# Kernel optimization log

Hardware: AMD Instinct MI355X
Metric: run time of the kernel (lower is better)

Reference implementation:

```python
import jax, jax.numpy as jnp
import numpy as np

B, N, E = 4, 2048, 512
H = 8
HD = E // H  # 64
SCALE = HD ** -0.5


def setup_inputs() -> dict:
    key = jax.random.key(0)
    k1, k2, k3 = jax.random.split(key, 3)
    x = jax.random.normal(k1, (B, N, E), dtype=jnp.float32)
    # xavier-uniform-like scaling for weights
    w_qkv = jax.random.normal(k2, (3 * E, E), dtype=jnp.float32) * (2.0 / (4 * E)) ** 0.5
    b_qkv = jnp.zeros((3 * E,), dtype=jnp.float32)
    w_out = jax.random.normal(k3, (E, E), dtype=jnp.float32) * (1.0 / E) ** 0.5
    b_out = jnp.zeros((E,), dtype=jnp.float32)
    return {"x": x, "w_qkv": w_qkv, "b_qkv": b_qkv, "w_out": w_out, "b_out": b_out}


def reference(x, w_qkv, b_qkv, w_out, b_out):
    b_sz, n_patches, _ = x.shape
    # qkv projection: [B,N,3E] -> [B,N,3,H,HD] -> [B,H,3,N,HD]
    qkv = (jnp.einsum('bne,fe->bnf', x, w_qkv) + b_qkv)
    qkv = qkv.reshape(b_sz, n_patches, 3, H, HD).transpose(0, 3, 2, 1, 4)
    q, k, v = qkv[:, :, 0], qkv[:, :, 1], qkv[:, :, 2]  # each [B,H,N,HD]
    attn = jnp.einsum('bhqd,bhkd->bhqk', q * SCALE, k)  # [B,H,N,N]
    attn = jax.nn.softmax(attn, axis=-1)
    # attn_dropout p=0.0 -> identity in reference
    out = jnp.einsum('bhqk,bhkd->bhqd', attn, v)  # [B,H,N,HD]
    out = out.transpose(0, 2, 1, 3).reshape(b_sz, n_patches, E)
    out = jnp.einsum('bne,fe->bnf', out, w_out) + b_out
    return out
```

## Files before the change

kernel.cpp:

```cpp
#include <hip/hip_runtime.h>

#define BB   4
#define SEQ  2048
#define EMB  512
#define NH   8
#define HD   64
#define QSCALE 0.18033688011f

typedef __bf16 bf16x8 __attribute__((ext_vector_type(8)));
typedef float  f32x4  __attribute__((ext_vector_type(4)));

__device__ __forceinline__ short f2bf(float f) {
  union { float f; unsigned u; } v; v.f = f;
  unsigned r = v.u + 0x7fffu + ((v.u >> 16) & 1u);
  return (short)(r >> 16);
}

__device__ __forceinline__ unsigned pk_bf16(float a, float b) {
#if __has_builtin(__builtin_amdgcn_cvt_pk_bf16_f32)
  typedef __bf16 bf16v2 __attribute__((ext_vector_type(2)));
  union { bf16v2 v; unsigned u; } cv;
  cv.v = __builtin_amdgcn_cvt_pk_bf16_f32(a, b);
  return cv.u;
#else
  return (unsigned)(unsigned short)f2bf(a) | ((unsigned)(unsigned short)f2bf(b) << 16);
#endif
}

__device__ __forceinline__ float fexp2(float x) {
#if __has_builtin(__builtin_amdgcn_exp2f)
  return __builtin_amdgcn_exp2f(x);
#else
  return exp2f(x);
#endif
}

__device__ __forceinline__ void gl_lds16(const void* g, void* l) {
  __builtin_amdgcn_global_load_lds(
      (const __attribute__((address_space(1))) unsigned int*)g,
      (__attribute__((address_space(3))) unsigned int*)l, 16, 0, 0);
}

__device__ __forceinline__ void quad_redist(unsigned &a, unsigned &b) {
  asm volatile("v_permlane32_swap_b32 %0, %1" : "+v"(a), "+v"(b));
  asm volatile("v_permlane16_swap_b32 %0, %1" : "+v"(a), "+v"(b));
}

__global__ __launch_bounds__(256) void cast_all(const float* __restrict__ x,
                                                const float* __restrict__ wq,
                                                const float* __restrict__ wo,
                                                short* __restrict__ xb,
                                                short* __restrict__ wqb,
                                                short* __restrict__ wob) {
  int i = blockIdx.x * 256 + threadIdx.x;
  const float* src; short* dst; int off;
  if (i < 1048576)      { src = x;  dst = xb;  off = i; }
  else if (i < 1245184) { src = wq; dst = wqb; off = i - 1048576; }
  else                  { src = wo; dst = wob; off = i - 1245184; }
  float4 v = ((const float4*)src)[off];
  uint2 o; o.x = pk_bf16(v.x, v.y); o.y = pk_bf16(v.z, v.w);
  *(uint2*)&dst[off * 4] = o;
}

__global__ __launch_bounds__(512, 6) void qkv_gemm(const short* __restrict__ A,
                                                   const short* __restrict__ W,
                                                   const float* __restrict__ bias,
                                                   short* __restrict__ qo,
                                                   short* __restrict__ ko,
                                                   short* __restrict__ vto) {
  __shared__ __align__(16) short As0[128 * 32];
  __shared__ __align__(16) short Bs0[128 * 32];
  __shared__ __align__(16) short As1[128 * 32];
  __shared__ __align__(16) short Bs1[128 * 32];
  const int tid  = threadIdx.x;
  const int lane = tid & 63, wave = tid >> 6;
  const int wm = wave >> 1, wf = wave & 1;
  const int col = lane & 15, quad = lane >> 4;
  const int m0 = blockIdx.x * 128, f0 = blockIdx.y * 128;

  const int row = tid >> 2;
  const int cb  = (tid & 3) ^ ((tid >> 3) & 3);
  const short* aSrc = A + (size_t)(m0 + row) * 512 + cb * 8;
  const short* wSrc = W + (size_t)(f0 + row) * 512 + cb * 8;

  const int rc = (quad ^ ((col >> 1) & 3)) * 8;
  int aOff[2], bOff[4];
#pragma unroll
  for (int i = 0; i < 2; ++i) aOff[i] = (wm * 32 + i * 16 + col) * 32 + rc;
#pragma unroll
  for (int j = 0; j < 4; ++j) bOff[j] = (wf * 64 + j * 16 + col) * 32 + rc;

  f32x4 acc[2][4];
#pragma unroll
  for (int i = 0; i < 2; ++i)
#pragma unroll
    for (int j = 0; j < 4; ++j)
#pragma unroll
      for (int r = 0; r < 4; ++r) acc[i][j][r] = 0.f;

#define QSTAGE(BUFA, BUFB, KS)                                        \
  {                                                                   \
    gl_lds16(aSrc + (KS) * 32, (char*)(BUFA) + wave * 1024);          \
    gl_lds16(wSrc + (KS) * 32, (char*)(BUFB) + wave * 1024);          \
  }

  auto qcompute = [&](const short* As, const short* Bs) {
    bf16x8 af[2], bw[4];
#pragma unroll
    for (int i = 0; i < 2; ++i) af[i] = *(const bf16x8*)&As[aOff[i]];
#pragma unroll
    for (int j = 0; j < 4; ++j) bw[j] = *(const bf16x8*)&Bs[bOff[j]];
#pragma unroll
    for (int i = 0; i < 2; ++i)
#pragma unroll
      for (int j = 0; j < 4; ++j)
        acc[i][j] = __builtin_amdgcn_mfma_f32_16x16x32_bf16(af[i], bw[j], acc[i][j], 0, 0, 0);
  };

  QSTAGE(As0, Bs0, 0);
  __syncthreads();
  for (int t = 0; t < 16; t += 2) {
    QSTAGE(As1, Bs1, t + 1);
    qcompute(As0, Bs0);
    __syncthreads();
    QSTAGE(As0, Bs0, (t + 2) & 15);
    qcompute(As1, Bs1);
    __syncthreads();
  }
#undef QSTAGE

#pragma unroll
  for (int j = 0; j < 4; ++j) {
    const int f = f0 + wf * 64 + j * 16 + col;
    const float bv = bias[f];
    const int sIdx = f >> 9;
    const int h = (f >> 6) & 7;
    const int d = f & 63;
#pragma unroll
    for (int i = 0; i < 2; ++i) {
      const int mbase = m0 + wm * 32 + i * 16 + quad * 4;
      const int b = mbase >> 11;
      const int n = mbase & 2047;
      const size_t bh = (size_t)(b * NH + h);
      if (sIdx == 2) {
        uint2 pk;
        pk.x = pk_bf16(acc[i][j][0] + bv, acc[i][j][1] + bv);
        pk.y = pk_bf16(acc[i][j][2] + bv, acc[i][j][3] + bv);
        *(uint2*)&vto[(bh * HD + d) * SEQ + n] = pk;
      } else if (sIdx == 0) {
#pragma unroll
        for (int r = 0; r < 4; ++r)
          qo[(bh * SEQ + n + r) * HD + d] = f2bf((acc[i][j][r] + bv) * QSCALE);
      } else {
#pragma unroll
        for (int r = 0; r < 4; ++r)
          ko[(bh * SEQ + n + r) * HD + d] = f2bf(acc[i][j][r] + bv);
      }
    }
  }
}

__global__ __launch_bounds__(512) void attn_kernel(const short* __restrict__ q,
                                                   const short* __restrict__ k,
                                                   const short* __restrict__ vt,
                                                   short* __restrict__ o) {
  __shared__ __align__(16) short Ks0[64 * 64];
  __shared__ __align__(16) short Vs0[64 * 64];
  __shared__ __align__(16) short Ks1[64 * 64];
  __shared__ __align__(16) short Vs1[64 * 64];

  const int tid  = threadIdx.x;
  const int lane = tid & 63, wave = tid >> 6;
  const int col = lane & 15, quad = lane >> 4;
  const int bh = blockIdx.x & 31;
  const int q0 = (blockIdx.x >> 5) * 128;
  const size_t bhBase = (size_t)bh * SEQ * HD;

  bf16x8 qf[2];
#pragma unroll
  for (int ks = 0; ks < 2; ++ks)
    qf[ks] = *(const bf16x8*)&q[bhBase +
        (size_t)(q0 + wave * 16 + col) * HD + ks * 32 + quad * 8];

  const int row = tid >> 3, cb = (tid & 7) ^ (row & 7);
  const short* ksrc = k  + bhBase + (size_t)row * HD  + cb * 8;
  const short* vsrc = vt + bhBase + (size_t)row * SEQ + cb * 8;
  char* const ldsK0 = (char*)Ks0 + wave * 1024;
  char* const ldsV0 = (char*)Vs0 + wave * 1024;
  char* const ldsK1 = (char*)Ks1 + wave * 1024;
  char* const ldsV1 = (char*)Vs1 + wave * 1024;

  f32x4 oacc[4];
#pragma unroll
  for (int nt = 0; nt < 4; ++nt)
#pragma unroll
    for (int r = 0; r < 4; ++r) oacc[nt][r] = 0.f;
  float lsum = 0.f;

  auto compute = [&](const short* KB, const short* VB) {
    f32x4 sacc[4];
#pragma unroll
    for (int kt = 0; kt < 4; ++kt)
#pragma unroll
      for (int r = 0; r < 4; ++r) sacc[kt][r] = 0.f;
#pragma unroll
    for (int ks = 0; ks < 2; ++ks)
#pragma unroll
      for (int kt = 0; kt < 4; ++kt) {
        bf16x8 kf = *(const bf16x8*)&KB[(kt * 16 + col) * 64 +
                                        (((ks * 4 + quad) ^ (col & 7)) * 8)];
        sacc[kt] = __builtin_amdgcn_mfma_f32_16x16x32_bf16(kf, qf[ks], sacc[kt], 0, 0, 0);
      }

    unsigned u[4][2];
#pragma unroll
    for (int kt = 0; kt < 4; ++kt) {
      float p0 = fexp2(sacc[kt][0]);
      float p1 = fexp2(sacc[kt][1]);
      float p2 = fexp2(sacc[kt][2]);
      float p3 = fexp2(sacc[kt][3]);
      lsum += (p0 + p1) + (p2 + p3);
      u[kt][0] = pk_bf16(p0, p1);
      u[kt][1] = pk_bf16(p2, p3);
    }

    union { unsigned w[4]; bf16x8 v; } pf0, pf1;
    {
      unsigned a, b;
      a = u[0][0]; b = u[1][0]; quad_redist(a, b); pf0.w[0] = a; pf0.w[2] = b;
      a = u[0][1]; b = u[1][1]; quad_redist(a, b); pf0.w[1] = a; pf0.w[3] = b;
      a = u[2][0]; b = u[3][0]; quad_redist(a, b); pf1.w[0] = a; pf1.w[2] = b;
      a = u[2][1]; b = u[3][1]; quad_redist(a, b); pf1.w[1] = a; pf1.w[3] = b;
    }

#pragma unroll
    for (int nt = 0; nt < 4; ++nt) {
      bf16x8 vf0 = *(const bf16x8*)&VB[(nt * 16 + col) * 64 +
                                       ((quad ^ (col & 7)) * 8)];
      oacc[nt] = __builtin_amdgcn_mfma_f32_16x16x32_bf16(pf0.v, vf0, oacc[nt], 0, 0, 0);
      bf16x8 vf1 = *(const bf16x8*)&VB[(nt * 16 + col) * 64 +
                                       (((4 + quad) ^ (col & 7)) * 8)];
      oacc[nt] = __builtin_amdgcn_mfma_f32_16x16x32_bf16(pf1.v, vf1, oacc[nt], 0, 0, 0);
    }
  };

  gl_lds16(ksrc, ldsK0); gl_lds16(vsrc, ldsV0);
  ksrc += 64 * HD; vsrc += 64;
  __syncthreads();

  for (int t = 0; t < 32; t += 2) {
    gl_lds16(ksrc, ldsK1); gl_lds16(vsrc, ldsV1);
    ksrc += 64 * HD; vsrc += 64;
    compute(Ks0, Vs0);
    __syncthreads();
    gl_lds16(ksrc, ldsK0); gl_lds16(vsrc, ldsV0);
    ksrc += 64 * HD; vsrc += 64;
    compute(Ks1, Vs1);
    __syncthreads();
  }

  lsum += __shfl_xor(lsum, 16);
  lsum += __shfl_xor(lsum, 32);

  const int b = bh >> 3, h = bh & 7;
#pragma unroll
  for (int r = 0; r < 4; ++r) {
    const float rl = 1.0f / __shfl(lsum, quad * 4 + r);
    const int n = q0 + wave * 16 + quad * 4 + r;
#pragma unroll
    for (int nt = 0; nt < 4; ++nt)
      o[((size_t)(b * SEQ + n)) * EMB + h * HD + nt * 16 + col] = f2bf(oacc[nt][r] * rl);
  }
}

__global__ __launch_bounds__(512, 4) void proj_gemm(const short* __restrict__ A,
                                                    const short* __restrict__ W,
                                                    const float* __restrict__ bias,
                                                    float* __restrict__ out) {
  __shared__ __align__(16) short As0[64 * 32];
  __shared__ __align__(16) short Bs0[128 * 32];
  __shared__ __align__(16) short As1[64 * 32];
  __shared__ __align__(16) short Bs1[128 * 32];
  const int tid  = threadIdx.x;
  const int lane = tid & 63, wave = tid >> 6;
  const int wm = wave >> 2, wf = wave & 3;
  const int col = lane & 15, quad = lane >> 4;
  const int m0 = blockIdx.x * 64, f0 = blockIdx.y * 128;

  const int aslot = tid & 255;
  const int arow = aslot >> 2, acb = (aslot & 3) ^ ((aslot >> 3) & 3);
  const short* aSrc = A + (size_t)(m0 + arow) * 512 + acb * 8;
  const int wrow = tid >> 2, wcb = (tid & 3) ^ ((tid >> 3) & 3);
  const short* wSrc = W + (size_t)(f0 + wrow) * 512 + wcb * 8;

  const int rc = (quad ^ ((col >> 1) & 3)) * 8;
  int aOff[2], bOff[2];
#pragma unroll
  for (int i = 0; i < 2; ++i) aOff[i] = (wm * 32 + i * 16 + col) * 32 + rc;
#pragma unroll
  for (int j = 0; j < 2; ++j) bOff[j] = (wf * 32 + j * 16 + col) * 32 + rc;

  f32x4 acc[2][2];
#pragma unroll
  for (int i = 0; i < 2; ++i)
#pragma unroll
    for (int j = 0; j < 2; ++j)
#pragma unroll
      for (int r = 0; r < 4; ++r) acc[i][j][r] = 0.f;

#define PSTAGE(BUFA, BUFB, KS)                                        \
  {                                                                   \
    if (wave < 4) gl_lds16(aSrc + (KS) * 32, (char*)(BUFA) + wave * 1024); \
    gl_lds16(wSrc + (KS) * 32, (char*)(BUFB) + wave * 1024);          \
  }

  auto pcompute = [&](const short* As, const short* Bs) {
    bf16x8 af[2], bw[2];
#pragma unroll
    for (int i = 0; i < 2; ++i) af[i] = *(const bf16x8*)&As[aOff[i]];
#pragma unroll
    for (int j = 0; j < 2; ++j) bw[j] = *(const bf16x8*)&Bs[bOff[j]];
#pragma unroll
    for (int i = 0; i < 2; ++i)
#pragma unroll
      for (int j = 0; j < 2; ++j)
        acc[i][j] = __builtin_amdgcn_mfma_f32_16x16x32_bf16(af[i], bw[j], acc[i][j], 0, 0, 0);
  };

  PSTAGE(As0, Bs0, 0);
  __syncthreads();
  for (int t = 0; t < 16; t += 2) {
    PSTAGE(As1, Bs1, t + 1);
    pcompute(As0, Bs0);
    __syncthreads();
    PSTAGE(As0, Bs0, (t + 2) & 15);
    pcompute(As1, Bs1);
    __syncthreads();
  }
#undef PSTAGE

#pragma unroll
  for (int j = 0; j < 2; ++j) {
    const int f = f0 + wf * 32 + j * 16 + col;
    const float bv = bias[f];
#pragma unroll
    for (int i = 0; i < 2; ++i) {
      const int mbase = m0 + wm * 32 + i * 16 + quad * 4;
#pragma unroll
      for (int r = 0; r < 4; ++r)
        out[(size_t)(mbase + r) * 512 + f] = acc[i][j][r] + bv;
    }
  }
}

extern "C" void kernel_launch(void* const* d_in, const int* in_sizes, int n_in,
                              void* d_out, int out_size, void* d_ws, size_t ws_size,
                              hipStream_t stream) {
  (void)in_sizes; (void)n_in; (void)out_size; (void)ws_size;
  const float* x     = (const float*)d_in[0];
  const float* w_qkv = (const float*)d_in[1];
  const float* b_qkv = (const float*)d_in[2];
  const float* w_out = (const float*)d_in[3];
  const float* b_out = (const float*)d_in[4];
  float* out = (float*)d_out;

  char* ws = (char*)d_ws;
  short* xb    = (short*)(ws + 0);
  short* wqkvb = (short*)(ws + 8388608);
  short* woutb = (short*)(ws + 9961472);
  short* qb    = (short*)(ws + 10485760);
  short* kb    = (short*)(ws + 18874368);
  short* vtb   = (short*)(ws + 27262976);
  short* ob    = (short*)(ws + 35651584);

  cast_all<<<5120, 256, 0, stream>>>(x, w_qkv, w_out, xb, wqkvb, woutb);
  qkv_gemm<<<dim3(64, 12), 512, 0, stream>>>(xb, wqkvb, b_qkv, qb, kb, vtb);
  attn_kernel<<<512, 512, 0, stream>>>(qb, kb, vtb, ob);
  proj_gemm<<<dim3(128, 4), 512, 0, stream>>>(ob, woutb, b_out, out);
}
```

Measured before the change: 153.8 us.

## Triple-buffer LDS in QKV and projection GEMMs with vmcnt-based waits

Replaces the double-buffered K loop in the qkv and output-projection GEMMs with a three-stage ring of LDS buffers. Two stages are prefetched, and each iteration waits only on the oldest outstanding global-to-LDS loads via explicit s_waitcnt vmcnt, then uses a single s_barrier. This keeps more loads in flight and drops one barrier per step. In exchange it uses more LDS per block, which may lower occupancy, and it depends on exact vmcnt bookkeeping for correctness.

```diff
diff --git a/kernel.cpp b/kernel.cpp
--- a/kernel.cpp
+++ b/kernel.cpp
@@ -68,10 +68,8 @@
                                                    short* __restrict__ qo,
                                                    short* __restrict__ ko,
                                                    short* __restrict__ vto) {
-  __shared__ __align__(16) short As0[128 * 32];
-  __shared__ __align__(16) short Bs0[128 * 32];
-  __shared__ __align__(16) short As1[128 * 32];
-  __shared__ __align__(16) short Bs1[128 * 32];
+  __shared__ __align__(16) short As[3][128 * 32];
+  __shared__ __align__(16) short Bs[3][128 * 32];
   const int tid  = threadIdx.x;
   const int lane = tid & 63, wave = tid >> 6;
   const int wm = wave >> 1, wf = wave & 1;
@@ -98,18 +96,18 @@
 #pragma unroll
       for (int r = 0; r < 4; ++r) acc[i][j][r] = 0.f;
 
-#define QSTAGE(BUFA, BUFB, KS)                                        \
+#define QSTAGE(BI, KS)                                                \
   {                                                                   \
-    gl_lds16(aSrc + (KS) * 32, (char*)(BUFA) + wave * 1024);          \
-    gl_lds16(wSrc + (KS) * 32, (char*)(BUFB) + wave * 1024);          \
-  }
-
-  auto qcompute = [&](const short* As, const short* Bs) {
+    gl_lds16(aSrc + (KS) * 32, (char*)As[BI] + wave * 1024);          \
+    gl_lds16(wSrc + (KS) * 32, (char*)Bs[BI] + wave * 1024);          \
+  }
+
+  auto qcompute = [&](const short* Asb, const short* Bsb) {
     bf16x8 af[2], bw[4];
 #pragma unroll
-    for (int i = 0; i < 2; ++i) af[i] = *(const bf16x8*)&As[aOff[i]];
-#pragma unroll
-    for (int j = 0; j < 4; ++j) bw[j] = *(const bf16x8*)&Bs[bOff[j]];
+    for (int i = 0; i < 2; ++i) af[i] = *(const bf16x8*)&Asb[aOff[i]];
+#pragma unroll
+    for (int j = 0; j < 4; ++j) bw[j] = *(const bf16x8*)&Bsb[bOff[j]];
 #pragma unroll
     for (int i = 0; i < 2; ++i)
 #pragma unroll
@@ -117,15 +115,16 @@
         acc[i][j] = __builtin_amdgcn_mfma_f32_16x16x32_bf16(af[i], bw[j], acc[i][j], 0, 0, 0);
   };
 
-  QSTAGE(As0, Bs0, 0);
-  __syncthreads();
-  for (int t = 0; t < 16; t += 2) {
-    QSTAGE(As1, Bs1, t + 1);
-    qcompute(As0, Bs0);
-    __syncthreads();
-    QSTAGE(As0, Bs0, (t + 2) & 15);
-    qcompute(As1, Bs1);
-    __syncthreads();
+  QSTAGE(0, 0);
+  QSTAGE(1, 1);
+#pragma unroll
+  for (int t = 0; t < 16; ++t) {
+    if (t < 15) { asm volatile("s_waitcnt vmcnt(2)" ::: "memory"); }
+    else        { asm volatile("s_waitcnt vmcnt(0)" ::: "memory"); }
+    __builtin_amdgcn_sched_barrier(0);
+    __builtin_amdgcn_s_barrier();
+    if (t + 2 < 16) QSTAGE((t + 2) % 3, t + 2);
+    qcompute(As[t % 3], Bs[t % 3]);
   }
 #undef QSTAGE
 
@@ -277,10 +276,8 @@
                                                     const short* __restrict__ W,
                                                     const float* __restrict__ bias,
                                                     float* __restrict__ out) {
-  __shared__ __align__(16) short As0[64 * 32];
-  __shared__ __align__(16) short Bs0[128 * 32];
-  __shared__ __align__(16) short As1[64 * 32];
-  __shared__ __align__(16) short Bs1[128 * 32];
+  __shared__ __align__(16) short As[3][64 * 32];
+  __shared__ __align__(16) short Bs[3][128 * 32];
   const int tid  = threadIdx.x;
   const int lane = tid & 63, wave = tid >> 6;
   const int wm = wave >> 2, wf = wave & 3;
@@ -308,18 +305,18 @@
 #pragma unroll
       for (int r = 0; r < 4; ++r) acc[i][j][r] = 0.f;
 
-#define PSTAGE(BUFA, BUFB, KS)                                        \
+#define PSTAGE(BI, KS)                                                \
   {                                                                   \
-    if (wave < 4) gl_lds16(aSrc + (KS) * 32, (char*)(BUFA) + wave * 1024); \
-    gl_lds16(wSrc + (KS) * 32, (char*)(BUFB) + wave * 1024);          \
-  }
-
-  auto pcompute = [&](const short* As, const short* Bs) {
+    if (wave < 4) gl_lds16(aSrc + (KS) * 32, (char*)As[BI] + wave * 1024); \
+    gl_lds16(wSrc + (KS) * 32, (char*)Bs[BI] + wave * 1024);          \
+  }
+
+  auto pcompute = [&](const short* Asb, const short* Bsb) {
     bf16x8 af[2], bw[2];
 #pragma unroll
-    for (int i = 0; i < 2; ++i) af[i] = *(const bf16x8*)&As[aOff[i]];
-#pragma unroll
-    for (int j = 0; j < 2; ++j) bw[j] = *(const bf16x8*)&Bs[bOff[j]];
+    for (int i = 0; i < 2; ++i) af[i] = *(const bf16x8*)&Asb[aOff[i]];
+#pragma unroll
+    for (int j = 0; j < 2; ++j) bw[j] = *(const bf16x8*)&Bsb[bOff[j]];
 #pragma unroll
     for (int i = 0; i < 2; ++i)
 #pragma unroll
@@ -327,15 +324,20 @@
         acc[i][j] = __builtin_amdgcn_mfma_f32_16x16x32_bf16(af[i], bw[j], acc[i][j], 0, 0, 0);
   };
 
-  PSTAGE(As0, Bs0, 0);
-  __syncthreads();
-  for (int t = 0; t < 16; t += 2) {
-    PSTAGE(As1, Bs1, t + 1);
-    pcompute(As0, Bs0);
-    __syncthreads();
-    PSTAGE(As0, Bs0, (t + 2) & 15);
-    pcompute(As1, Bs1);
-    __syncthreads();
+  PSTAGE(0, 0);
+  PSTAGE(1, 1);
+#pragma unroll
+  for (int t = 0; t < 16; ++t) {
+    if (t < 15) {
+      if (wave < 4) { asm volatile("s_waitcnt vmcnt(2)" ::: "memory"); }
+      else          { asm volatile("s_waitcnt vmcnt(1)" ::: "memory"); }
+    } else {
+      asm volatile("s_waitcnt vmcnt(0)" ::: "memory");
+    }
+    __builtin_amdgcn_sched_barrier(0);
+    __builtin_amdgcn_s_barrier();
+    if (t + 2 < 16) PSTAGE((t + 2) % 3, t + 2);
+    pcompute(As[t % 3], Bs[t % 3]);
   }
 #undef PSTAGE
 
```

Result: no change. 155.1 us (+0.9%).

## Switch attention to 32x32x16 MFMA with split-KV waves and LDS reduction

Applied to the files above, without the earlier changes.

Rewrites the attention inner loop to use 32x32x16 bf16 MFMA tiles instead of 16x16x32. Each pair of waves shares a 32-row query group and splits each 64-key tile between them. The partial outputs and row sums are combined through LDS at the end. The aim is fewer MFMA and LDS fragment loads per useful FLOP and simpler permlane redistribution, at the cost of an extra cross-wave reduction and a higher occupancy hint.

```diff
diff --git a/kernel.cpp b/kernel.cpp
--- a/kernel.cpp
+++ b/kernel.cpp
@@ -9,6 +9,7 @@
 
 typedef __bf16 bf16x8 __attribute__((ext_vector_type(8)));
 typedef float  f32x4  __attribute__((ext_vector_type(4)));
+typedef float  f32x16 __attribute__((ext_vector_type(16)));
 
 __device__ __forceinline__ short f2bf(float f) {
   union { float f; unsigned u; } v; v.f = f;
@@ -41,9 +42,8 @@
       (__attribute__((address_space(3))) unsigned int*)l, 16, 0, 0);
 }
 
-__device__ __forceinline__ void quad_redist(unsigned &a, unsigned &b) {
+__device__ __forceinline__ void swap32(unsigned &a, unsigned &b) {
   asm volatile("v_permlane32_swap_b32 %0, %1" : "+v"(a), "+v"(b));
-  asm volatile("v_permlane16_swap_b32 %0, %1" : "+v"(a), "+v"(b));
 }
 
 __global__ __launch_bounds__(256) void cast_all(const float* __restrict__ x,
@@ -160,88 +160,82 @@
   }
 }
 
-__global__ __launch_bounds__(512) void attn_kernel(const short* __restrict__ q,
-                                                   const short* __restrict__ k,
-                                                   const short* __restrict__ vt,
-                                                   short* __restrict__ o) {
-  __shared__ __align__(16) short Ks0[64 * 64];
-  __shared__ __align__(16) short Vs0[64 * 64];
-  __shared__ __align__(16) short Ks1[64 * 64];
-  __shared__ __align__(16) short Vs1[64 * 64];
+__global__ __launch_bounds__(512, 4) void attn_kernel(const short* __restrict__ q,
+                                                      const short* __restrict__ k,
+                                                      const short* __restrict__ vt,
+                                                      short* __restrict__ o) {
+  __shared__ __align__(16) short KV[4][64 * 64];
+  __shared__ float Ls[4][32];
 
   const int tid  = threadIdx.x;
   const int lane = tid & 63, wave = tid >> 6;
-  const int col = lane & 15, quad = lane >> 4;
+  const int l31 = lane & 31, g = lane >> 5;
+  const int qg = wave >> 1, kh = wave & 1;
   const int bh = blockIdx.x & 31;
   const int q0 = (blockIdx.x >> 5) * 128;
   const size_t bhBase = (size_t)bh * SEQ * HD;
 
-  bf16x8 qf[2];
-#pragma unroll
-  for (int ks = 0; ks < 2; ++ks)
+  bf16x8 qf[4];
+#pragma unroll
+  for (int ks = 0; ks < 4; ++ks)
     qf[ks] = *(const bf16x8*)&q[bhBase +
-        (size_t)(q0 + wave * 16 + col) * HD + ks * 32 + quad * 8];
+        (size_t)(q0 + qg * 32 + l31) * HD + ks * 16 + g * 8];
 
   const int row = tid >> 3, cb = (tid & 7) ^ (row & 7);
   const short* ksrc = k  + bhBase + (size_t)row * HD  + cb * 8;
   const short* vsrc = vt + bhBase + (size_t)row * SEQ + cb * 8;
-  char* const ldsK0 = (char*)Ks0 + wave * 1024;
-  char* const ldsV0 = (char*)Vs0 + wave * 1024;
-  char* const ldsK1 = (char*)Ks1 + wave * 1024;
-  char* const ldsV1 = (char*)Vs1 + wave * 1024;
-
-  f32x4 oacc[4];
-#pragma unroll
-  for (int nt = 0; nt < 4; ++nt)
-#pragma unroll
-    for (int r = 0; r < 4; ++r) oacc[nt][r] = 0.f;
+  char* const ldsK0 = (char*)KV[0] + wave * 1024;
+  char* const ldsV0 = (char*)KV[1] + wave * 1024;
+  char* const ldsK1 = (char*)KV[2] + wave * 1024;
+  char* const ldsV1 = (char*)KV[3] + wave * 1024;
+
+  f32x16 oacc[2];
+#pragma unroll
+  for (int nt = 0; nt < 2; ++nt)
+#pragma unroll
+    for (int r = 0; r < 16; ++r) oacc[nt][r] = 0.f;
   float lsum = 0.f;
 
+  const int krow = kh * 32 + l31;
+  const int kx   = krow & 7;
+
   auto compute = [&](const short* KB, const short* VB) {
-    f32x4 sacc[4];
-#pragma unroll
-    for (int kt = 0; kt < 4; ++kt)
-#pragma unroll
-      for (int r = 0; r < 4; ++r) sacc[kt][r] = 0.f;
-#pragma unroll
-    for (int ks = 0; ks < 2; ++ks)
-#pragma unroll
-      for (int kt = 0; kt < 4; ++kt) {
-        bf16x8 kf = *(const bf16x8*)&KB[(kt * 16 + col) * 64 +
-                                        (((ks * 4 + quad) ^ (col & 7)) * 8)];
-        sacc[kt] = __builtin_amdgcn_mfma_f32_16x16x32_bf16(kf, qf[ks], sacc[kt], 0, 0, 0);
-      }
-
+    f32x16 sacc;
+#pragma unroll
+    for (int r = 0; r < 16; ++r) sacc[r] = 0.f;
+#pragma unroll
+    for (int ks = 0; ks < 4; ++ks) {
+      bf16x8 kf = *(const bf16x8*)&KB[krow * 64 + (((ks * 2 + g) ^ kx) * 8)];
+      sacc = __builtin_amdgcn_mfma_f32_32x32x16_bf16(kf, qf[ks], sacc, 0, 0, 0);
+    }
     unsigned u[4][2];
 #pragma unroll
-    for (int kt = 0; kt < 4; ++kt) {
-      float p0 = fexp2(sacc[kt][0]);
-      float p1 = fexp2(sacc[kt][1]);
-      float p2 = fexp2(sacc[kt][2]);
-      float p3 = fexp2(sacc[kt][3]);
+    for (int hi = 0; hi < 4; ++hi) {
+      float p0 = fexp2(sacc[4 * hi + 0]);
+      float p1 = fexp2(sacc[4 * hi + 1]);
+      float p2 = fexp2(sacc[4 * hi + 2]);
+      float p3 = fexp2(sacc[4 * hi + 3]);
       lsum += (p0 + p1) + (p2 + p3);
-      u[kt][0] = pk_bf16(p0, p1);
-      u[kt][1] = pk_bf16(p2, p3);
-    }
-
-    union { unsigned w[4]; bf16x8 v; } pf0, pf1;
+      u[hi][0] = pk_bf16(p0, p1);
+      u[hi][1] = pk_bf16(p2, p3);
+    }
+    union { unsigned w[4]; bf16x8 v; } pf[2];
     {
       unsigned a, b;
-      a = u[0][0]; b = u[1][0]; quad_redist(a, b); pf0.w[0] = a; pf0.w[2] = b;
-      a = u[0][1]; b = u[1][1]; quad_redist(a, b); pf0.w[1] = a; pf0.w[3] = b;
-      a = u[2][0]; b = u[3][0]; quad_redist(a, b); pf1.w[0] = a; pf1.w[2] = b;
-      a = u[2][1]; b = u[3][1]; quad_redist(a, b); pf1.w[1] = a; pf1.w[3] = b;
-    }
-
-#pragma unroll
-    for (int nt = 0; nt < 4; ++nt) {
-      bf16x8 vf0 = *(const bf16x8*)&VB[(nt * 16 + col) * 64 +
-                                       ((quad ^ (col & 7)) * 8)];
-      oacc[nt] = __builtin_amdgcn_mfma_f32_16x16x32_bf16(pf0.v, vf0, oacc[nt], 0, 0, 0);
-      bf16x8 vf1 = *(const bf16x8*)&VB[(nt * 16 + col) * 64 +
-                                       (((4 + quad) ^ (col & 7)) * 8)];
-      oacc[nt] = __builtin_amdgcn_mfma_f32_16x16x32_bf16(pf1.v, vf1, oacc[nt], 0, 0, 0);
-    }
+      a = u[0][0]; b = u[1][0]; swap32(a, b); pf[0].w[0] = a; pf[0].w[2] = b;
+      a = u[0][1]; b = u[1][1]; swap32(a, b); pf[0].w[1] = a; pf[0].w[3] = b;
+      a = u[2][0]; b = u[3][0]; swap32(a, b); pf[1].w[0] = a; pf[1].w[2] = b;
+      a = u[2][1]; b = u[3][1]; swap32(a, b); pf[1].w[1] = a; pf[1].w[3] = b;
+    }
+#pragma unroll
+    for (int km = 0; km < 2; ++km)
+#pragma unroll
+      for (int nt = 0; nt < 2; ++nt) {
+        const int vrow = nt * 32 + l31;
+        bf16x8 vf = *(const bf16x8*)&VB[vrow * 64 +
+                                        (((kh * 4 + km * 2 + g) ^ (vrow & 7)) * 8)];
+        oacc[nt] = __builtin_amdgcn_mfma_f32_32x32x16_bf16(pf[km].v, vf, oacc[nt], 0, 0, 0);
+      }
   };
 
   gl_lds16(ksrc, ldsK0); gl_lds16(vsrc, ldsV0);
@@ -251,25 +245,44 @@
   for (int t = 0; t < 32; t += 2) {
     gl_lds16(ksrc, ldsK1); gl_lds16(vsrc, ldsV1);
     ksrc += 64 * HD; vsrc += 64;
-    compute(Ks0, Vs0);
+    compute((const short*)KV[0], (const short*)KV[1]);
     __syncthreads();
     gl_lds16(ksrc, ldsK0); gl_lds16(vsrc, ldsV0);
     ksrc += 64 * HD; vsrc += 64;
-    compute(Ks1, Vs1);
-    __syncthreads();
-  }
-
-  lsum += __shfl_xor(lsum, 16);
+    compute((const short*)KV[2], (const short*)KV[3]);
+    __syncthreads();
+  }
+
   lsum += __shfl_xor(lsum, 32);
-
-  const int b = bh >> 3, h = bh & 7;
-#pragma unroll
-  for (int r = 0; r < 4; ++r) {
-    const float rl = 1.0f / __shfl(lsum, quad * 4 + r);
-    const int n = q0 + wave * 16 + quad * 4 + r;
-#pragma unroll
-    for (int nt = 0; nt < 4; ++nt)
-      o[((size_t)(b * SEQ + n)) * EMB + h * HD + nt * 16 + col] = f2bf(oacc[nt][r] * rl);
+  float* M = (float*)KV;
+  if (kh == 1) {
+#pragma unroll
+    for (int nt = 0; nt < 2; ++nt)
+#pragma unroll
+      for (int r = 0; r < 16; ++r) {
+        const int idx = nt * 16 + r;
+        M[qg * 2048 + lane * 32 + ((idx + lane) & 31)] = oacc[nt][r];
+      }
+    if (lane < 32) Ls[qg][l31] = lsum;
+  }
+  __syncthreads();
+  if (kh == 0) {
+    const float inv = 1.0f / (lsum + Ls[qg][l31]);
+    const int b = bh >> 3, h = bh & 7;
+    float rl[16];
+#pragma unroll
+    for (int r = 0; r < 16; ++r)
+      rl[r] = __shfl(inv, (r & 3) + 8 * (r >> 2) + 4 * g);
+#pragma unroll
+    for (int nt = 0; nt < 2; ++nt)
+#pragma unroll
+      for (int r = 0; r < 16; ++r) {
+        const int idx = nt * 16 + r;
+        const float val = (oacc[nt][r] +
+                           M[qg * 2048 + lane * 32 + ((idx + lane) & 31)]) * rl[r];
+        const int n = q0 + qg * 32 + (r & 3) + 8 * (r >> 2) + 4 * g;
+        o[((size_t)(b * SEQ + n)) * EMB + h * HD + nt * 32 + l31] = f2bf(val);
+      }
   }
 }
 
```

After: 155.8 us. No clear change (+1.3%).
